# Kernel tuning notes

Hardware: AMD Instinct MI355X
Metric: run time of the kernel (lower is better)

The kernel has to match this reference:

```python
import jax, jax.numpy as jnp
import numpy as np

B, S, DIM = 2, 2048, 2048
N_HEADS, N_KV_HEADS = 16, 4
HEAD_DIM = DIM // N_HEADS  # 128
N_REP = N_HEADS // N_KV_HEADS  # 4
ROPE_THETA = 10000.0


def setup_inputs() -> dict:
    key = jax.random.key(0)
    ks = jax.random.split(key, 6)
    x = jax.random.normal(ks[0], (B, S, DIM), dtype=jnp.float32)
    # torch nn.Linear weights are [out_features, in_features]
    sc = 0.02
    wq = jax.random.normal(ks[1], (N_HEADS * HEAD_DIM, DIM), dtype=jnp.float32) * sc
    wk = jax.random.normal(ks[2], (N_KV_HEADS * HEAD_DIM, DIM), dtype=jnp.float32) * sc
    wv = jax.random.normal(ks[3], (N_KV_HEADS * HEAD_DIM, DIM), dtype=jnp.float32) * sc
    wo = jax.random.normal(ks[4], (DIM, N_HEADS * HEAD_DIM), dtype=jnp.float32) * sc
    # precomputed rotary table (freqs_cis in llama): [S, head_dim//2]
    inv_freq = 1.0 / (ROPE_THETA ** (jnp.arange(0, HEAD_DIM, 2, dtype=jnp.float32) / HEAD_DIM))
    t = jnp.arange(S, dtype=jnp.float32)
    freqs = jnp.outer(t, inv_freq)  # [S, head_dim//2]
    freqs_cos = jnp.cos(freqs)
    freqs_sin = jnp.sin(freqs)
    # additive causal mask as passed to SDPA (float, 0 on allowed, -inf-like elsewhere)
    causal = jnp.tril(jnp.ones((S, S), dtype=bool))
    mask = jnp.where(causal, 0.0, -1e9).astype(jnp.float32)
    return {"x": x, "wq": wq, "wk": wk, "wv": wv, "wo": wo,
            "freqs_cos": freqs_cos, "freqs_sin": freqs_sin, "mask": mask}


def _apply_rope(t, cos, sin):
    # t: [B, S, H, D]; cos/sin: [S, D//2] -> complex multiply on adjacent pairs
    tr = t.reshape(*t.shape[:-1], -1, 2)  # [B,S,H,D/2,2]
    tre, tim = tr[..., 0], tr[..., 1]
    c = cos[None, :, None, :]
    s = sin[None, :, None, :]
    out_re = tre * c - tim * s
    out_im = tre * s + tim * c
    return jnp.stack([out_re, out_im], axis=-1).reshape(t.shape)


def reference(x, wq, wk, wv, wo, freqs_cos, freqs_sin, mask):
    Bx, Sx, _ = x.shape
    xq = (x @ wq.T).reshape(Bx, Sx, N_HEADS, HEAD_DIM)
    xk = (x @ wk.T).reshape(Bx, Sx, N_KV_HEADS, HEAD_DIM)
    xv = (x @ wv.T).reshape(Bx, Sx, N_KV_HEADS, HEAD_DIM)
    xq = _apply_rope(xq, freqs_cos, freqs_sin)
    xk = _apply_rope(xk, freqs_cos, freqs_sin)
    # repeat_kv for GQA: [B,S,KV,D] -> [B,S,KV*n_rep,D]
    keys = jnp.repeat(xk, N_REP, axis=2)
    values = jnp.repeat(xv, N_REP, axis=2)
    q = xq.transpose(0, 2, 1, 3)      # [B,H,S,D]
    k = keys.transpose(0, 2, 1, 3)
    v = values.transpose(0, 2, 1, 3)
    scale = 1.0 / jnp.sqrt(jnp.float32(HEAD_DIM))
    scores = jnp.einsum('bhqd,bhkd->bhqk', q, k) * scale + mask[None, None]
    attn = jax.nn.softmax(scores, axis=-1)
    out = jnp.einsum('bhqk,bhkd->bhqd', attn, v)
    out = out.transpose(0, 2, 1, 3).reshape(Bx, Sx, -1)
    return out @ wo.T
```

## Files before the change

### kernel.cpp

```cpp
#include <hip/hip_runtime.h>
#include <hip/hip_bf16.h>

#define B_   2
#define S_   2048
#define DIM_ 2048
#define NH   16
#define NKV  4
#define HD   128
#define QKVN 3072

typedef __attribute__((ext_vector_type(8)))  short  sv8;
typedef __attribute__((ext_vector_type(8)))  ushort usv8;
typedef __attribute__((ext_vector_type(4)))  float  fv4;
typedef __attribute__((ext_vector_type(16))) float  fv16;

__device__ __forceinline__ float fast_exp2(float x) {
  return __builtin_amdgcn_exp2f(x);
}

__device__ __forceinline__ ushort f2bf(float f) {
  __hip_bfloat16 h = __float2bfloat16(f);
  union { __hip_bfloat16 h; ushort u; } c; c.h = h; return c.u;
}
__device__ __forceinline__ float bf2f(ushort u) {
  union { unsigned int i; float f; } c; c.i = ((unsigned)u) << 16; return c.f;
}

__device__ __forceinline__ unsigned int cvtpk(float lo, float hi) {
  unsigned int r;
  asm("v_cvt_pk_bf16_f32 %0, %1, %2" : "=v"(r) : "v"(lo), "v"(hi));
  return r;
}
__device__ __forceinline__ unsigned int xhalf(unsigned int x) {
  return (unsigned int)__shfl_xor((int)x, 32, 64);
}

__device__ __forceinline__ float tmax16(const fv16& v) {
  float a = fmaxf(fmaxf(v[0], v[1]),  fmaxf(v[2], v[3]));
  float b = fmaxf(fmaxf(v[4], v[5]),  fmaxf(v[6], v[7]));
  float c = fmaxf(fmaxf(v[8], v[9]),  fmaxf(v[10], v[11]));
  float d = fmaxf(fmaxf(v[12], v[13]), fmaxf(v[14], v[15]));
  return fmaxf(fmaxf(a, b), fmaxf(c, d));
}
__device__ __forceinline__ float tsum16(const fv16& v) {
  float a = (v[0] + v[1]) + (v[2] + v[3]);
  float b = (v[4] + v[5]) + (v[6] + v[7]);
  float c = (v[8] + v[9]) + (v[10] + v[11]);
  float d = (v[12] + v[13]) + (v[14] + v[15]);
  return (a + b) + (c + d);
}

__device__ __forceinline__ void async16(const void* g, void* l) {
  __builtin_amdgcn_global_load_lds(
      (const __attribute__((address_space(1))) unsigned int*)g,
      (__attribute__((address_space(3))) unsigned int*)l, 16, 0, 0);
}

__global__ void cvt_kernel(const float* __restrict__ in, ushort* __restrict__ out, int n) {
  int i = (blockIdx.x * 256 + threadIdx.x) * 4;
  if (i >= n) return;
  fv4 v = *(const fv4*)(in + i);
  ushort4 o;
  o.x = f2bf(v[0]); o.y = f2bf(v[1]); o.z = f2bf(v[2]); o.w = f2bf(v[3]);
  *(ushort4*)(out + i) = o;
}

__global__ void cvtw_kernel(const float* __restrict__ wq, const float* __restrict__ wk,
                            const float* __restrict__ wv, const float* __restrict__ wo,
                            ushort* __restrict__ wqkvb, ushort* __restrict__ wob) {
  const int NQ = 2048 * 2048, NK = 512 * 2048;
  int i = (blockIdx.x * 256 + threadIdx.x) * 4;
  const float* src; ushort* dst;
  if (i < NQ)               { src = wq + i;                 dst = wqkvb + i; }
  else if (i < NQ + NK)     { src = wk + (i - NQ);          dst = wqkvb + i; }
  else if (i < NQ + 2 * NK) { src = wv + (i - NQ - NK);     dst = wqkvb + i; }
  else                      { int j = i - (NQ + 2 * NK); src = wo + j; dst = wob + j; }
  fv4 v = *(const fv4*)src;
  ushort4 o;
  o.x = f2bf(v[0]); o.y = f2bf(v[1]); o.z = f2bf(v[2]); o.w = f2bf(v[3]);
  *(ushort4*)dst = o;
}

__global__ void rope2_kernel(const ushort* __restrict__ qkv, const float* __restrict__ fc,
                             const float* __restrict__ fs, ushort* __restrict__ qr,
                             ushort* __restrict__ kr, float qscale) {
  int t = blockIdx.x * 256 + threadIdx.x;
  int grp = t & 15;
  int u   = t >> 4;
  int h2  = u % 20;
  int s   = (u / 20) % S_;
  int b   = u / (20 * S_);
  bool isQ  = h2 < 16;
  int h     = isQ ? h2 : h2 - 16;
  int heads = isQ ? NH : NKV;
  float scale = isQ ? qscale : 1.0f;
  const ushort* src = qkv + (size_t)(b * S_ + s) * QKVN + (isQ ? 0 : 2048) + h * HD + grp * 8;
  sv8 v = *(const sv8*)src;
  fv4 c  = *(const fv4*)(fc + s * 64 + grp * 4);
  fv4 sn = *(const fv4*)(fs + s * 64 + grp * 4);
  sv8 o;
#pragma unroll
  for (int p = 0; p < 4; ++p) {
    float re = bf2f((ushort)v[2 * p]);
    float im = bf2f((ushort)v[2 * p + 1]);
    float orr = (re * c[p] - im * sn[p]) * scale;
    float oi  = (re * sn[p] + im * c[p]) * scale;
    o[2 * p]     = (short)f2bf(orr);
    o[2 * p + 1] = (short)f2bf(oi);
  }
  ushort* dst = (isQ ? qr : kr) + ((size_t)(b * heads + h) * S_ + s) * HD + grp * 8;
  *(sv8*)dst = o;
}

__global__ __launch_bounds__(256) void vtrans_kernel(const ushort* __restrict__ vraw,
                                                     ushort* __restrict__ vt, int rowstride) {
  __shared__ ushort tile[128][136];
  int blk = blockIdx.x;
  int st  = blk & 15;
  int kvb = blk >> 4;
  int kv  = kvb & 3;
  int b   = kvb >> 2;
  int s0  = st << 7;
#pragma unroll
  for (int it = 0; it < 8; ++it) {
    int t = it * 256 + threadIdx.x;
    int srow = t >> 4;
    int d8 = (t & 15) * 8;
    usv8 v = *(const usv8*)(vraw + (size_t)(b * S_ + s0 + srow) * rowstride + kv * HD + d8);
#pragma unroll
    for (int j = 0; j < 8; ++j) tile[d8 + j][srow] = v[j];
  }
  __syncthreads();
#pragma unroll
  for (int it = 0; it < 8; ++it) {
    int t = it * 256 + threadIdx.x;
    int d = t >> 4;
    int s8 = (t & 15) * 8;
    usv8 o;
#pragma unroll
    for (int j = 0; j < 8; ++j) o[j] = tile[d][s8 + j];
    *(usv8*)(vt + ((size_t)(b * NKV + kv) * HD + d) * S_ + s0 + s8) = o;
  }
}

template <typename OutT>
__global__ __launch_bounds__(512) void gemm192(const ushort* __restrict__ A,
                                               const ushort* __restrict__ Bm,
                                               OutT* __restrict__ C,
                                               int M, int N, int K) {
  __shared__ __align__(16) ushort SM[57344];
  int nb = N / 192;
  int bx = blockIdx.x % nb, by = blockIdx.x / nb;
  int m0 = by << 8;
  int n0 = bx * 192;
  int tid = threadIdx.x;
  int lane = tid & 63, w = tid >> 6;
  int l15 = lane & 15, lg = lane >> 4;
  int wm = (w >> 2) * 128;
  int wn = (w & 3) * 48;
  int pA = w >> 2;

  int srow = tid >> 3;
  int cb   = ((tid & 7) * 16) ^ ((srow & 7) << 4);
  const ushort* sA = A  + (size_t)(m0 + srow) * K + (cb >> 1);
  const ushort* sB = Bm + (size_t)(n0 + srow) * K + (cb >> 1);
  size_t rstep = (size_t)64 * K;
  int nkt = K >> 6;

  auto STG_A = [&](int t, int db) {
    ushort* base = SM + db * 28672 + (w << 9);
    const ushort* a0 = sA + (size_t)t * 64;
    async16(a0,             base);
    async16(a0 + rstep,     base + 4096);
    async16(a0 + 2 * rstep, base + 8192);
    async16(a0 + 3 * rstep, base + 12288);
  };
  auto STG_B = [&](int t, int db) {
    ushort* base = SM + db * 28672 + 16384 + (w << 9);
    const ushort* b0 = sB + (size_t)t * 64;
    async16(b0,             base);
    async16(b0 + rstep,     base + 4096);
    async16(b0 + 2 * rstep, base + 8192);
  };

  fv4 acc[8][3] = {};
  sv8 alo[4][2], ahi[4][2], b01[2][2], b2v[2];

  STG_A(0, 0); STG_B(0, 0);
  { int t1 = nkt > 1 ? 1 : 0; STG_A(t1, 1); STG_B(t1, 1); }
  asm volatile("s_waitcnt vmcnt(7)");
  __builtin_amdgcn_s_barrier();

  for (int t = 0; t < nkt; ++t) {
    int db = t & 1;
    int t2 = t + 2 < nkt ? t + 2 : nkt - 1;
    const char* Ab = (const char*)(SM + db * 28672) + pA * 16384;
    const char* Bb = (const char*)(SM + db * 28672) + 32768;

#pragma unroll
    for (int m = 0; m < 4; ++m)
#pragma unroll
      for (int kk = 0; kk < 2; ++kk) {
        int row = m * 16 + l15;
        alo[m][kk] = *(const sv8*)(Ab + row * 128 + ((kk * 64 + lg * 16) ^ ((row & 7) << 4)));
      }
#pragma unroll
    for (int m = 0; m < 4; ++m)
#pragma unroll
      for (int kk = 0; kk < 2; ++kk) {
        int row = 64 + m * 16 + l15;
        ahi[m][kk] = *(const sv8*)(Ab + row * 128 + ((kk * 64 + lg * 16) ^ ((row & 7) << 4)));
      }
#pragma unroll
    for (int j = 0; j < 2; ++j)
#pragma unroll
      for (int kk = 0; kk < 2; ++kk) {
        int row = wn + j * 16 + l15;
        b01[j][kk] = *(const sv8*)(Bb + row * 128 + ((kk * 64 + lg * 16) ^ ((row & 7) << 4)));
      }
#pragma unroll
    for (int kk = 0; kk < 2; ++kk) {
      int row = wn + 32 + l15;
      b2v[kk] = *(const sv8*)(Bb + row * 128 + ((kk * 64 + lg * 16) ^ ((row & 7) << 4)));
    }
    __builtin_amdgcn_s_barrier();
    asm volatile("s_waitcnt lgkmcnt(0)");
    __builtin_amdgcn_s_setprio(1);
#pragma unroll
    for (int m = 0; m < 4; ++m)
#pragma unroll
      for (int j = 0; j < 2; ++j)
#pragma unroll
        for (int kk = 0; kk < 2; ++kk) {
          acc[m][j]     = __builtin_amdgcn_mfma_f32_16x16x32_bf16(alo[m][kk], b01[j][kk], acc[m][j], 0, 0, 0);
          acc[m + 4][j] = __builtin_amdgcn_mfma_f32_16x16x32_bf16(ahi[m][kk], b01[j][kk], acc[m + 4][j], 0, 0, 0);
        }
    __builtin_amdgcn_s_setprio(0);
    __builtin_amdgcn_s_barrier();

    STG_A(t2, db);
    STG_B(t2, db);
    asm volatile("s_waitcnt vmcnt(7)");
    __builtin_amdgcn_s_barrier();
    __builtin_amdgcn_s_setprio(1);
#pragma unroll
    for (int m = 0; m < 4; ++m)
#pragma unroll
      for (int kk = 0; kk < 2; ++kk) {
        acc[m][2]     = __builtin_amdgcn_mfma_f32_16x16x32_bf16(alo[m][kk], b2v[kk], acc[m][2], 0, 0, 0);
        acc[m + 4][2] = __builtin_amdgcn_mfma_f32_16x16x32_bf16(ahi[m][kk], b2v[kk], acc[m + 4][2], 0, 0, 0);
      }
    __builtin_amdgcn_s_setprio(0);
    __builtin_amdgcn_s_barrier();
  }

  asm volatile("s_waitcnt vmcnt(0)");
#pragma unroll
  for (int m = 0; m < 8; ++m)
#pragma unroll
    for (int j = 0; j < 3; ++j)
#pragma unroll
      for (int r = 0; r < 4; ++r) {
        int row = m0 + wm + m * 16 + lg * 4 + r;
        int col = n0 + wn + j * 16 + l15;
        if constexpr (sizeof(OutT) == 2) C[(size_t)row * N + col] = (OutT)f2bf(acc[m][j][r]);
        else                             C[(size_t)row * N + col] = (OutT)acc[m][j][r];
      }
}

template <typename OutT>
__global__ __launch_bounds__(512) void gemmOP(const ushort* __restrict__ A,
                                              const ushort* __restrict__ Bm,
                                              OutT* __restrict__ C,
                                              int M, int N, int K) {
  __shared__ __align__(16) ushort SM[49152];
  int nb = N >> 7;
  int bx = blockIdx.x % nb, by = blockIdx.x / nb;
  int m0 = by << 8, n0 = bx << 7;
  int tid = threadIdx.x;
  int lane = tid & 63, w = tid >> 6;
  int l15 = lane & 15, lg = lane >> 4;
  int wm = (w >> 2) * 128;
  int wn = (w & 3) * 32;
  int pA = (w >> 2);

  int srow = tid >> 3;
  int cb   = ((tid & 7) * 16) ^ ((srow & 7) << 4);
  const ushort* sA0 = A  + (size_t)(m0 + srow) * K + (cb >> 1);
  const ushort* sB0 = Bm + (size_t)(n0 + srow) * K + (cb >> 1);
  const ushort* srcs[3] = { sA0, sA0 + (size_t)128 * K, sB0 };
  size_t rstep = (size_t)64 * K;

  int nkt = K >> 6;

  auto STG = [&](int part, int t, int db) {
    ushort* d0 = SM + db * 24576 + part * 8192 + (w << 9);
    const ushort* s0 = srcs[part] + t * 64;
    async16(s0, d0);
    async16(s0 + rstep, d0 + 4096);
  };

  fv4 acc[8][2] = {};
  sv8 a[8][2], b[2][2];

#pragma unroll
  for (int p = 0; p < 3; ++p) STG(p, 0, 0);
  {
    int t1 = 1 < nkt ? 1 : 0;
#pragma unroll
    for (int p = 0; p < 3; ++p) STG(p, t1, 1);
  }
  asm volatile("s_waitcnt vmcnt(6)");
  __builtin_amdgcn_s_barrier();

  for (int t = 0; t < nkt; ++t) {
    int db = t & 1;
    int t2 = t + 2 < nkt ? t + 2 : nkt - 1;
    const char* Ab = (const char*)SM + db * 49152 + pA * 16384;
    const char* Bb = (const char*)SM + db * 49152 + 32768;

#pragma unroll
    for (int m = 0; m < 8; ++m)
#pragma unroll
      for (int kk = 0; kk < 2; ++kk) {
        int row = m * 16 + l15;
        a[m][kk] = *(const sv8*)(Ab + row * 128 + ((kk * 64 + lg * 16) ^ ((row & 7) << 4)));
      }
#pragma unroll
    for (int j = 0; j < 2; ++j)
#pragma unroll
      for (int kk = 0; kk < 2; ++kk) {
        int row = wn + j * 16 + l15;
        b[j][kk] = *(const sv8*)(Bb + row * 128 + ((kk * 64 + lg * 16) ^ ((row & 7) << 4)));
      }
    __builtin_amdgcn_s_barrier();
    asm volatile("s_waitcnt lgkmcnt(0)");
    __builtin_amdgcn_s_setprio(1);
#pragma unroll
    for (int m = 0; m < 4; ++m)
#pragma unroll
      for (int j = 0; j < 2; ++j)
#pragma unroll
        for (int kk = 0; kk < 2; ++kk)
          acc[m][j] = __builtin_amdgcn_mfma_f32_16x16x32_bf16(a[m][kk], b[j][kk], acc[m][j], 0, 0, 0);
    __builtin_amdgcn_s_setprio(0);
    __builtin_amdgcn_s_barrier();

    STG(0, t2, db);
    STG(1, t2, db);
    STG(2, t2, db);
    asm volatile("s_waitcnt vmcnt(6)");
    __builtin_amdgcn_s_barrier();
    __builtin_amdgcn_s_setprio(1);
#pragma unroll
    for (int m = 0; m < 4; ++m)
#pragma unroll
      for (int j = 0; j < 2; ++j)
#pragma unroll
        for (int kk = 0; kk < 2; ++kk)
          acc[m + 4][j] = __builtin_amdgcn_mfma_f32_16x16x32_bf16(a[m + 4][kk], b[j][kk], acc[m + 4][j], 0, 0, 0);
    __builtin_amdgcn_s_setprio(0);
    __builtin_amdgcn_s_barrier();
  }

  asm volatile("s_waitcnt vmcnt(0)");
#pragma unroll
  for (int m = 0; m < 8; ++m)
#pragma unroll
    for (int j = 0; j < 2; ++j)
#pragma unroll
      for (int r = 0; r < 4; ++r) {
        int row = m0 + wm + m * 16 + lg * 4 + r;
        int col = n0 + wn + j * 16 + l15;
        if constexpr (sizeof(OutT) == 2) C[(size_t)row * N + col] = (OutT)f2bf(acc[m][j][r]);
        else                             C[(size_t)row * N + col] = (OutT)acc[m][j][r];
      }
}

__global__ __launch_bounds__(512, 2) void attn_kernel(const ushort* __restrict__ Q,
                                                      const ushort* __restrict__ Kr,
                                                      const ushort* __restrict__ Vt,
                                                      ushort* __restrict__ O) {
  __shared__ __align__(16) ushort SMEM[65536];

  int blk = blockIdx.x;
  int bh  = blk & 31;
  int pr  = blk >> 5;
  int h   = bh & 15;
  int b   = bh >> 4;
  int kv  = h >> 2;
  int lane = threadIdx.x & 63, w = threadIdx.x >> 6;
  int wg = w & 3, Hf = w >> 2;
  int l31 = lane & 31, hh = lane >> 5;

  const ushort* Qbase = Q  + (size_t)(b * NH  + h ) * S_ * HD;
  const ushort* Kbase = Kr + (size_t)(b * NKV + kv) * S_ * HD;
  const ushort* Vbase = Vt + (size_t)(b * NKV + kv) * HD * S_;

  const ushort* kSrc[4]; ushort* kDst[2][4];
  const ushort* vSrc[4]; ushort* vDst[2][4];
#pragma unroll
  for (int it = 0; it < 4; ++it) {
    int lin = it * 4096 + wg * 1024 + lane * 16;
    { int row = lin >> 8; int cbv = (lin & 255) ^ ((row & 15) << 4);
      kSrc[it] = Kbase + (size_t)row * HD + (cbv >> 1); }
    { int row = lin >> 8; int cp = lin & 255; int cl = cp ^ ((row & 15) << 4);
      int d = row + ((cl >> 7) << 6);
      int koff = (cl & 127) >> 1;
      vSrc[it] = Vbase + (size_t)d * S_ + koff; }
#pragma unroll
    for (int buf = 0; buf < 2; ++buf) {
      kDst[buf][it] = SMEM + Hf * 16384 + buf * 8192 + ((it * 4096 + wg * 1024) >> 1);
      vDst[buf][it] = SMEM + 32768 + Hf * 16384 + buf * 8192 + ((it * 4096 + wg * 1024) >> 1);
    }
  }

  float* cML = (float*)SMEM;
  float* cO  = (float*)SMEM + 512;

  for (int pass = 0; pass < 2; ++pass) {
    int qt = pass ? (15 - pr) : pr;
    int q0 = qt << 7;
    int qrow_w = q0 + wg * 32;
    int myq    = qrow_w + l31;
    int nj     = qt + 1;
    int ktbase = Hf * nj;

    sv8 qf[8];
#pragma unroll
    for (int kk = 0; kk < 8; ++kk)
      qf[kk] = *(const sv8*)(Qbase + (size_t)myq * HD + kk * 16 + hh * 8);

    fv16 oacc[4] = {};
    float mrun = -1e30f, lrun = 0.f;

    {
      size_t k0 = (size_t)ktbase << 6;
#pragma unroll
      for (int it = 0; it < 4; ++it) async16(kSrc[it] + k0 * HD, kDst[0][it]);
#pragma unroll
      for (int it = 0; it < 4; ++it) async16(vSrc[it] + k0,      vDst[0][it]);
    }

    for (int j = 0; j < nj; ++j) {
      int cur = j & 1, nxt = cur ^ 1;
      __syncthreads();
      if (j + 1 < nj) {
        size_t k0n = (size_t)(ktbase + j + 1) << 6;
#pragma unroll
        for (int it = 0; it < 4; ++it) async16(kSrc[it] + k0n * HD, kDst[nxt][it]);
#pragma unroll
        for (int it = 0; it < 4; ++it) async16(vSrc[it] + k0n,      vDst[nxt][it]);
      }
      const char* KsC = (const char*)(SMEM + Hf * 16384 + cur * 8192);
      const char* VsC = (const char*)(SMEM + 32768 + Hf * 16384 + cur * 8192);
      int k0 = (ktbase + j) << 6;

      fv16 sacc[2] = {};
      __builtin_amdgcn_s_setprio(1);
#pragma unroll
      for (int kk = 0; kk < 8; ++kk) {
        int cbq = kk * 32 + hh * 16;
        int r0 = l31, r1 = 32 + l31;
        sv8 kf0 = *(const sv8*)(KsC + r0 * 256 + (cbq ^ ((r0 & 15) << 4)));
        sv8 kf1 = *(const sv8*)(KsC + r1 * 256 + (cbq ^ ((r1 & 15) << 4)));
        sacc[0] = __builtin_amdgcn_mfma_f32_32x32x16_bf16(kf0, qf[kk], sacc[0], 0, 0, 0);
        sacc[1] = __builtin_amdgcn_mfma_f32_32x32x16_bf16(kf1, qf[kk], sacc[1], 0, 0, 0);
      }
      __builtin_amdgcn_s_setprio(0);

      if (k0 + 63 > qrow_w) {
        int thr = myq - k0 - 4 * hh;
#pragma unroll
        for (int t = 0; t < 2; ++t)
#pragma unroll
          for (int r = 0; r < 16; ++r) {
            int kp = t * 32 + (r & 3) + 8 * (r >> 2);
            if (kp > thr) sacc[t][r] = -1e38f;
          }
      }

      float tmax = fmaxf(tmax16(sacc[0]), tmax16(sacc[1]));
      tmax = fmaxf(tmax, __shfl_xor(tmax, 32, 64));

      if (__any(tmax > mrun + 8.0f)) {
        float mnew = fmaxf(mrun, tmax);
        float esc  = fast_exp2(mrun - mnew);
        lrun *= esc;
        float er[16];
#pragma unroll
        for (int r = 0; r < 16; ++r) er[r] = __shfl(esc, (r & 3) + 8 * (r >> 2) + 4 * hh, 64);
#pragma unroll
        for (int d0 = 0; d0 < 4; ++d0)
#pragma unroll
          for (int r = 0; r < 16; ++r) oacc[d0][r] *= er[r];
        mrun = mnew;
      }

#pragma unroll
      for (int t = 0; t < 2; ++t)
#pragma unroll
        for (int r = 0; r < 16; ++r) sacc[t][r] = fast_exp2(sacc[t][r] - mrun);
      float psum = tsum16(sacc[0]) + tsum16(sacc[1]);
      psum += __shfl_xor(psum, 32, 64);
      lrun += psum;

      union Frag { unsigned int u[4]; sv8 v; } pa[4];
#pragma unroll
      for (int t = 0; t < 2; ++t)
#pragma unroll
        for (int half = 0; half < 2; ++half) {
          int cbq = half * 8;
          unsigned int a0 = cvtpk(sacc[t][cbq + 0], sacc[t][cbq + 1]);
          unsigned int a1 = cvtpk(sacc[t][cbq + 2], sacc[t][cbq + 3]);
          unsigned int b0 = cvtpk(sacc[t][cbq + 4], sacc[t][cbq + 5]);
          unsigned int b1 = cvtpk(sacc[t][cbq + 6], sacc[t][cbq + 7]);
          unsigned int a0p = xhalf(a0), a1p = xhalf(a1);
          unsigned int b0p = xhalf(b0), b1p = xhalf(b1);
          pa[2 * t + half].u[0] = hh ? b0p : a0;
          pa[2 * t + half].u[1] = hh ? b1p : a1;
          pa[2 * t + half].u[2] = hh ? b0  : a0p;
          pa[2 * t + half].u[3] = hh ? b1  : a1p;
        }

      __builtin_amdgcn_s_setprio(1);
#pragma unroll
      for (int ks = 0; ks < 4; ++ks) {
#pragma unroll
        for (int d0 = 0; d0 < 4; ++d0) {
          int d = d0 * 32 + l31;
          int row = d & 63;
          int cl = ((d >> 6) << 7) + ks * 32 + hh * 16;
          sv8 vf = *(const sv8*)(VsC + row * 256 + (cl ^ ((row & 15) << 4)));
          oacc[d0] = __builtin_amdgcn_mfma_f32_32x32x16_bf16(pa[ks].v, vf, oacc[d0], 0, 0, 0);
        }
      }
      __builtin_amdgcn_s_setprio(0);
    }

    __syncthreads();
    if (Hf) {
      int base = wg * 64 + lane;
      cML[base * 2]     = mrun;
      cML[base * 2 + 1] = lrun;
      float* dst = cO + base * 65;
#pragma unroll
      for (int d0 = 0; d0 < 4; ++d0)
#pragma unroll
        for (int r = 0; r < 16; ++r) dst[d0 * 16 + r] = oacc[d0][r];
    }
    __syncthreads();
    if (!Hf) {
      int base = wg * 64 + lane;
      float m2 = cML[base * 2], l2 = cML[base * 2 + 1];
      const float* src = cO + base * 65;
      float m  = fmaxf(mrun, m2);
      float e1 = fast_exp2(mrun - m), e2 = fast_exp2(m2 - m);
      float l  = lrun * e1 + l2 * e2;
      float inv = 1.0f / l;
      float f1 = e1 * inv, f2 = e2 * inv;
      float f1b[16], f2b[16];
#pragma unroll
      for (int r = 0; r < 16; ++r) {
        int ro = (r & 3) + 8 * (r >> 2) + 4 * hh;
        f1b[r] = __shfl(f1, ro, 64);
        f2b[r] = __shfl(f2, ro, 64);
      }
#pragma unroll
      for (int r = 0; r < 16; ++r) {
        int q = qrow_w + (r & 3) + 8 * (r >> 2) + 4 * hh;
#pragma unroll
        for (int d0 = 0; d0 < 4; ++d0) {
          int d = d0 * 32 + l31;
          float val = oacc[d0][r] * f1b[r] + src[d0 * 16 + r] * f2b[r];
          O[(size_t)(b * S_ + q) * DIM_ + h * HD + d] = f2bf(val);
        }
      }
    }
    __syncthreads();
  }
}

extern "C" void kernel_launch(void* const* d_in, const int* in_sizes, int n_in,
                              void* d_out, int out_size, void* d_ws, size_t ws_size,
                              hipStream_t stream) {
  const float* x  = (const float*)d_in[0];
  const float* wq = (const float*)d_in[1];
  const float* wk = (const float*)d_in[2];
  const float* wv = (const float*)d_in[3];
  const float* wo = (const float*)d_in[4];
  const float* fc = (const float*)d_in[5];
  const float* fs = (const float*)d_in[6];
  float* out = (float*)d_out;

  char* ws = (char*)d_ws;
  size_t off = 0;
  auto alloc = [&](size_t bytes) -> ushort* {
    ushort* p = (ushort*)(ws + off);
    off += (bytes + 255) & ~(size_t)255;
    return p;
  };
  ushort* xb    = alloc((size_t)B_ * S_ * DIM_ * 2);
  ushort* wqkvb = alloc((size_t)QKVN * DIM_ * 2);
  ushort* wob   = alloc((size_t)DIM_ * DIM_ * 2);
  ushort* qkvr  = alloc((size_t)B_ * S_ * QKVN * 2);
  ushort* qr    = alloc((size_t)B_ * S_ * DIM_ * 2);
  ushort* kr    = alloc((size_t)B_ * S_ * NKV * HD * 2);
  ushort* vtb   = alloc((size_t)B_ * S_ * NKV * HD * 2);
  ushort* obf   = alloc((size_t)B_ * S_ * DIM_ * 2);
  (void)ws_size; (void)n_in; (void)in_sizes; (void)out_size;

  cvt_kernel<<<(B_ * S_ * DIM_) / 1024, 256, 0, stream>>>(x, xb, B_ * S_ * DIM_);
  cvtw_kernel<<<(2 * DIM_ * DIM_ + 2 * NKV * HD * DIM_) / 1024, 256, 0, stream>>>(
      wq, wk, wv, wo, wqkvb, wob);

  gemm192<ushort><<<(B_ * S_ / 256) * (QKVN / 192), 512, 0, stream>>>(xb, wqkvb, qkvr,
                                                                     B_ * S_, QKVN, DIM_);

  const float qscale = 0.08838834764831845f * 1.4426950408889634f;
  rope2_kernel<<<(B_ * S_ * 20 * 16) / 256, 256, 0, stream>>>(qkvr, fc, fs, qr, kr, qscale);
  vtrans_kernel<<<B_ * NKV * (S_ / 128), 256, 0, stream>>>(qkvr + 2560, vtb, QKVN);

  attn_kernel<<<B_ * NH * 8, 512, 0, stream>>>(qr, kr, vtb, obf);

  gemmOP<float><<<(B_ * S_ / 256) * (DIM_ / 128), 512, 0, stream>>>(obf, wob, out, B_ * S_, DIM_, DIM_);
}
```

Baseline: 186.2 us.

## Split heavy causal query tiles across blocks with atomic-counter global combine

```diff
diff --git a/kernel.cpp b/kernel.cpp
--- a/kernel.cpp
+++ b/kernel.cpp
@@ -377,21 +377,42 @@
       }
 }
 
-__global__ __launch_bounds__(512, 2) void attn_kernel(const ushort* __restrict__ Q,
+__global__ __launch_bounds__(256, 2) void attn_kernel(const ushort* __restrict__ Q,
                                                       const ushort* __restrict__ Kr,
                                                       const ushort* __restrict__ Vt,
-                                                      ushort* __restrict__ O) {
-  __shared__ __align__(16) ushort SMEM[65536];
-
-  int blk = blockIdx.x;
-  int bh  = blk & 31;
-  int pr  = blk >> 5;
+                                                      ushort* __restrict__ O,
+                                                      float* __restrict__ pOf,
+                                                      float* __restrict__ pML,
+                                                      int* __restrict__ cnt) {
+  __shared__ __align__(16) ushort SMEM[32768];
+  __shared__ int oldS;
+
+  int bid = blockIdx.x;
+  bool split = bid < 512;
+  int hf, key, qt, bh;
+  if (split) {
+    hf  = bid & 1;
+    key = bid >> 1;
+    bh  = key & 31;
+    qt  = 15 - (key >> 5);
+  } else {
+    hf  = 0;
+    key = 0;
+    int s = bid - 512;
+    bh  = s & 31;
+    qt  = 7 - (s >> 5);
+  }
   int h   = bh & 15;
   int b   = bh >> 4;
   int kv  = h >> 2;
-  int lane = threadIdx.x & 63, w = threadIdx.x >> 6;
-  int wg = w & 3, Hf = w >> 2;
+  int tid = threadIdx.x;
+  int lane = tid & 63, w = tid >> 6;
   int l31 = lane & 31, hh = lane >> 5;
+  int q0 = qt << 7;
+  int qrow_w = q0 + w * 32;
+  int myq    = qrow_w + l31;
+  int nj     = split ? (qt + 1) : (2 * qt + 2);
+  int ktbase = split ? hf * nj : 0;
 
   const ushort* Qbase = Q  + (size_t)(b * NH  + h ) * S_ * HD;
   const ushort* Kbase = Kr + (size_t)(b * NKV + kv) * S_ * HD;
@@ -401,7 +422,7 @@
   const ushort* vSrc[4]; ushort* vDst[2][4];
 #pragma unroll
   for (int it = 0; it < 4; ++it) {
-    int lin = it * 4096 + wg * 1024 + lane * 16;
+    int lin = it * 4096 + w * 1024 + lane * 16;
     { int row = lin >> 8; int cbv = (lin & 255) ^ ((row & 15) << 4);
       kSrc[it] = Kbase + (size_t)row * HD + (cbv >> 1); }
     { int row = lin >> 8; int cp = lin & 255; int cl = cp ^ ((row & 15) << 4);
@@ -410,174 +431,194 @@
       vSrc[it] = Vbase + (size_t)d * S_ + koff; }
 #pragma unroll
     for (int buf = 0; buf < 2; ++buf) {
-      kDst[buf][it] = SMEM + Hf * 16384 + buf * 8192 + ((it * 4096 + wg * 1024) >> 1);
-      vDst[buf][it] = SMEM + 32768 + Hf * 16384 + buf * 8192 + ((it * 4096 + wg * 1024) >> 1);
-    }
-  }
-
-  float* cML = (float*)SMEM;
-  float* cO  = (float*)SMEM + 512;
-
-  for (int pass = 0; pass < 2; ++pass) {
-    int qt = pass ? (15 - pr) : pr;
-    int q0 = qt << 7;
-    int qrow_w = q0 + wg * 32;
-    int myq    = qrow_w + l31;
-    int nj     = qt + 1;
-    int ktbase = Hf * nj;
-
-    sv8 qf[8];
-#pragma unroll
-    for (int kk = 0; kk < 8; ++kk)
-      qf[kk] = *(const sv8*)(Qbase + (size_t)myq * HD + kk * 16 + hh * 8);
-
-    fv16 oacc[4] = {};
-    float mrun = -1e30f, lrun = 0.f;
-
-    {
-      size_t k0 = (size_t)ktbase << 6;
-#pragma unroll
-      for (int it = 0; it < 4; ++it) async16(kSrc[it] + k0 * HD, kDst[0][it]);
-#pragma unroll
-      for (int it = 0; it < 4; ++it) async16(vSrc[it] + k0,      vDst[0][it]);
-    }
-
-    for (int j = 0; j < nj; ++j) {
-      int cur = j & 1, nxt = cur ^ 1;
-      __syncthreads();
-      if (j + 1 < nj) {
-        size_t k0n = (size_t)(ktbase + j + 1) << 6;
-#pragma unroll
-        for (int it = 0; it < 4; ++it) async16(kSrc[it] + k0n * HD, kDst[nxt][it]);
-#pragma unroll
-        for (int it = 0; it < 4; ++it) async16(vSrc[it] + k0n,      vDst[nxt][it]);
-      }
-      const char* KsC = (const char*)(SMEM + Hf * 16384 + cur * 8192);
-      const char* VsC = (const char*)(SMEM + 32768 + Hf * 16384 + cur * 8192);
-      int k0 = (ktbase + j) << 6;
-
-      fv16 sacc[2] = {};
-      __builtin_amdgcn_s_setprio(1);
-#pragma unroll
-      for (int kk = 0; kk < 8; ++kk) {
-        int cbq = kk * 32 + hh * 16;
-        int r0 = l31, r1 = 32 + l31;
-        sv8 kf0 = *(const sv8*)(KsC + r0 * 256 + (cbq ^ ((r0 & 15) << 4)));
-        sv8 kf1 = *(const sv8*)(KsC + r1 * 256 + (cbq ^ ((r1 & 15) << 4)));
-        sacc[0] = __builtin_amdgcn_mfma_f32_32x32x16_bf16(kf0, qf[kk], sacc[0], 0, 0, 0);
-        sacc[1] = __builtin_amdgcn_mfma_f32_32x32x16_bf16(kf1, qf[kk], sacc[1], 0, 0, 0);
-      }
-      __builtin_amdgcn_s_setprio(0);
-
-      if (k0 + 63 > qrow_w) {
-        int thr = myq - k0 - 4 * hh;
-#pragma unroll
-        for (int t = 0; t < 2; ++t)
-#pragma unroll
-          for (int r = 0; r < 16; ++r) {
-            int kp = t * 32 + (r & 3) + 8 * (r >> 2);
-            if (kp > thr) sacc[t][r] = -1e38f;
-          }
-      }
-
-      float tmax = fmaxf(tmax16(sacc[0]), tmax16(sacc[1]));
-      tmax = fmaxf(tmax, __shfl_xor(tmax, 32, 64));
-
-      if (__any(tmax > mrun + 8.0f)) {
-        float mnew = fmaxf(mrun, tmax);
-        float esc  = fast_exp2(mrun - mnew);
-        lrun *= esc;
-        float er[16];
-#pragma unroll
-        for (int r = 0; r < 16; ++r) er[r] = __shfl(esc, (r & 3) + 8 * (r >> 2) + 4 * hh, 64);
-#pragma unroll
-        for (int d0 = 0; d0 < 4; ++d0)
-#pragma unroll
-          for (int r = 0; r < 16; ++r) oacc[d0][r] *= er[r];
-        mrun = mnew;
-      }
-
+      kDst[buf][it] = SMEM + buf * 8192 + ((it * 4096 + w * 1024) >> 1);
+      vDst[buf][it] = SMEM + 16384 + buf * 8192 + ((it * 4096 + w * 1024) >> 1);
+    }
+  }
+
+  sv8 qf[8];
+#pragma unroll
+  for (int kk = 0; kk < 8; ++kk)
+    qf[kk] = *(const sv8*)(Qbase + (size_t)myq * HD + kk * 16 + hh * 8);
+
+  fv16 oacc[4] = {};
+  float mrun = -1e30f, lrun = 0.f;
+
+  {
+    size_t k0 = (size_t)ktbase << 6;
+#pragma unroll
+    for (int it = 0; it < 4; ++it) async16(kSrc[it] + k0 * HD, kDst[0][it]);
+#pragma unroll
+    for (int it = 0; it < 4; ++it) async16(vSrc[it] + k0,      vDst[0][it]);
+  }
+
+  for (int j = 0; j < nj; ++j) {
+    int cur = j & 1, nxt = cur ^ 1;
+    __syncthreads();
+    if (j + 1 < nj) {
+      size_t k0n = (size_t)(ktbase + j + 1) << 6;
+#pragma unroll
+      for (int it = 0; it < 4; ++it) async16(kSrc[it] + k0n * HD, kDst[nxt][it]);
+#pragma unroll
+      for (int it = 0; it < 4; ++it) async16(vSrc[it] + k0n,      vDst[nxt][it]);
+    }
+    const char* KsC = (const char*)(SMEM + cur * 8192);
+    const char* VsC = (const char*)(SMEM + 16384 + cur * 8192);
+    int k0 = (ktbase + j) << 6;
+
+    fv16 sacc[2] = {};
+    __builtin_amdgcn_s_setprio(1);
+#pragma unroll
+    for (int kk = 0; kk < 8; ++kk) {
+      int cbq = kk * 32 + hh * 16;
+      int r0 = l31, r1 = 32 + l31;
+      sv8 kf0 = *(const sv8*)(KsC + r0 * 256 + (cbq ^ ((r0 & 15) << 4)));
+      sv8 kf1 = *(const sv8*)(KsC + r1 * 256 + (cbq ^ ((r1 & 15) << 4)));
+      sacc[0] = __builtin_amdgcn_mfma_f32_32x32x16_bf16(kf0, qf[kk], sacc[0], 0, 0, 0);
+      sacc[1] = __builtin_amdgcn_mfma_f32_32x32x16_bf16(kf1, qf[kk], sacc[1], 0, 0, 0);
+    }
+    __builtin_amdgcn_s_setprio(0);
+
+    if (k0 + 63 > qrow_w) {
+      int thr = myq - k0 - 4 * hh;
 #pragma unroll
       for (int t = 0; t < 2; ++t)
 #pragma unroll
-        for (int r = 0; r < 16; ++r) sacc[t][r] = fast_exp2(sacc[t][r] - mrun);
-      float psum = tsum16(sacc[0]) + tsum16(sacc[1]);
-      psum += __shfl_xor(psum, 32, 64);
-      lrun += psum;
-
-      union Frag { unsigned int u[4]; sv8 v; } pa[4];
-#pragma unroll
-      for (int t = 0; t < 2; ++t)
-#pragma unroll
-        for (int half = 0; half < 2; ++half) {
-          int cbq = half * 8;
-          unsigned int a0 = cvtpk(sacc[t][cbq + 0], sacc[t][cbq + 1]);
-          unsigned int a1 = cvtpk(sacc[t][cbq + 2], sacc[t][cbq + 3]);
-          unsigned int b0 = cvtpk(sacc[t][cbq + 4], sacc[t][cbq + 5]);
-          unsigned int b1 = cvtpk(sacc[t][cbq + 6], sacc[t][cbq + 7]);
-          unsigned int a0p = xhalf(a0), a1p = xhalf(a1);
-          unsigned int b0p = xhalf(b0), b1p = xhalf(b1);
-          pa[2 * t + half].u[0] = hh ? b0p : a0;
-          pa[2 * t + half].u[1] = hh ? b1p : a1;
-          pa[2 * t + half].u[2] = hh ? b0  : a0p;
-          pa[2 * t + half].u[3] = hh ? b1  : a1p;
+        for (int r = 0; r < 16; ++r) {
+          int kp = t * 32 + (r & 3) + 8 * (r >> 2);
+          if (kp > thr) sacc[t][r] = -1e38f;
         }
-
-      __builtin_amdgcn_s_setprio(1);
-#pragma unroll
-      for (int ks = 0; ks < 4; ++ks) {
-#pragma unroll
-        for (int d0 = 0; d0 < 4; ++d0) {
-          int d = d0 * 32 + l31;
-          int row = d & 63;
-          int cl = ((d >> 6) << 7) + ks * 32 + hh * 16;
-          sv8 vf = *(const sv8*)(VsC + row * 256 + (cl ^ ((row & 15) << 4)));
-          oacc[d0] = __builtin_amdgcn_mfma_f32_32x32x16_bf16(pa[ks].v, vf, oacc[d0], 0, 0, 0);
-        }
-      }
-      __builtin_amdgcn_s_setprio(0);
-    }
-
-    __syncthreads();
-    if (Hf) {
-      int base = wg * 64 + lane;
-      cML[base * 2]     = mrun;
-      cML[base * 2 + 1] = lrun;
-      float* dst = cO + base * 65;
+    }
+
+    float tmax = fmaxf(tmax16(sacc[0]), tmax16(sacc[1]));
+    tmax = fmaxf(tmax, __shfl_xor(tmax, 32, 64));
+
+    if (__any(tmax > mrun + 8.0f)) {
+      float mnew = fmaxf(mrun, tmax);
+      float esc  = fast_exp2(mrun - mnew);
+      lrun *= esc;
+      float er[16];
+#pragma unroll
+      for (int r = 0; r < 16; ++r) er[r] = __shfl(esc, (r & 3) + 8 * (r >> 2) + 4 * hh, 64);
 #pragma unroll
       for (int d0 = 0; d0 < 4; ++d0)
 #pragma unroll
-        for (int r = 0; r < 16; ++r) dst[d0 * 16 + r] = oacc[d0][r];
-    }
-    __syncthreads();
-    if (!Hf) {
-      int base = wg * 64 + lane;
-      float m2 = cML[base * 2], l2 = cML[base * 2 + 1];
-      const float* src = cO + base * 65;
-      float m  = fmaxf(mrun, m2);
-      float e1 = fast_exp2(mrun - m), e2 = fast_exp2(m2 - m);
-      float l  = lrun * e1 + l2 * e2;
-      float inv = 1.0f / l;
-      float f1 = e1 * inv, f2 = e2 * inv;
-      float f1b[16], f2b[16];
-#pragma unroll
-      for (int r = 0; r < 16; ++r) {
-        int ro = (r & 3) + 8 * (r >> 2) + 4 * hh;
-        f1b[r] = __shfl(f1, ro, 64);
-        f2b[r] = __shfl(f2, ro, 64);
-      }
-#pragma unroll
-      for (int r = 0; r < 16; ++r) {
+        for (int r = 0; r < 16; ++r) oacc[d0][r] *= er[r];
+      mrun = mnew;
+    }
+
+#pragma unroll
+    for (int t = 0; t < 2; ++t)
+#pragma unroll
+      for (int r = 0; r < 16; ++r) sacc[t][r] = fast_exp2(sacc[t][r] - mrun);
+    float psum = tsum16(sacc[0]) + tsum16(sacc[1]);
+    psum += __shfl_xor(psum, 32, 64);
+    lrun += psum;
+
+    union Frag { unsigned int u[4]; sv8 v; } pa[4];
+#pragma unroll
+    for (int t = 0; t < 2; ++t)
+#pragma unroll
+      for (int half = 0; half < 2; ++half) {
+        int cbq = half * 8;
+        unsigned int a0 = cvtpk(sacc[t][cbq + 0], sacc[t][cbq + 1]);
+        unsigned int a1 = cvtpk(sacc[t][cbq + 2], sacc[t][cbq + 3]);
+        unsigned int b0 = cvtpk(sacc[t][cbq + 4], sacc[t][cbq + 5]);
+        unsigned int b1 = cvtpk(sacc[t][cbq + 6], sacc[t][cbq + 7]);
+        unsigned int a0p = xhalf(a0), a1p = xhalf(a1);
+        unsigned int b0p = xhalf(b0), b1p = xhalf(b1);
+        pa[2 * t + half].u[0] = hh ? b0p : a0;
+        pa[2 * t + half].u[1] = hh ? b1p : a1;
+        pa[2 * t + half].u[2] = hh ? b0  : a0p;
+        pa[2 * t + half].u[3] = hh ? b1  : a1p;
+      }
+
+    __builtin_amdgcn_s_setprio(1);
+#pragma unroll
+    for (int ks = 0; ks < 4; ++ks) {
+#pragma unroll
+      for (int d0 = 0; d0 < 4; ++d0) {
+        int d = d0 * 32 + l31;
+        int row = d & 63;
+        int cl = ((d >> 6) << 7) + ks * 32 + hh * 16;
+        sv8 vf = *(const sv8*)(VsC + row * 256 + (cl ^ ((row & 15) << 4)));
+        oacc[d0] = __builtin_amdgcn_mfma_f32_32x32x16_bf16(pa[ks].v, vf, oacc[d0], 0, 0, 0);
+      }
+    }
+    __builtin_amdgcn_s_setprio(0);
+  }
+
+  if (!split) {
+    float inv = 1.0f / lrun;
+    float ir[16];
+#pragma unroll
+    for (int r = 0; r < 16; ++r) ir[r] = __shfl(inv, (r & 3) + 8 * (r >> 2) + 4 * hh, 64);
+#pragma unroll
+    for (int r = 0; r < 16; ++r) {
+      int q = qrow_w + (r & 3) + 8 * (r >> 2) + 4 * hh;
+#pragma unroll
+      for (int d0 = 0; d0 < 4; ++d0) {
+        int d = d0 * 32 + l31;
+        O[(size_t)(b * S_ + q) * DIM_ + h * HD + d] = f2bf(oacc[d0][r] * ir[r]);
+      }
+    }
+    return;
+  }
+
+  {
+    float* myO = pOf + ((size_t)key * 2 + hf) * 16384 + (size_t)tid * 64;
+#pragma unroll
+    for (int d0 = 0; d0 < 4; ++d0)
+#pragma unroll
+      for (int j2 = 0; j2 < 4; ++j2) {
+        fv4 t;
+        t[0] = oacc[d0][4 * j2 + 0]; t[1] = oacc[d0][4 * j2 + 1];
+        t[2] = oacc[d0][4 * j2 + 2]; t[3] = oacc[d0][4 * j2 + 3];
+        *(fv4*)(myO + d0 * 16 + 4 * j2) = t;
+      }
+    float* myML = pML + ((size_t)key * 2 + hf) * 512 + tid * 2;
+    myML[0] = mrun;
+    myML[1] = lrun;
+  }
+  __threadfence();
+  __syncthreads();
+  if (tid == 0) oldS = atomicAdd(&cnt[key], 1);
+  __syncthreads();
+  if (oldS == 0) return;
+  __threadfence();
+
+  const float* o0 = pOf + (size_t)key * 32768 + (size_t)tid * 64;
+  const float* o1 = o0 + 16384;
+  const float* ml0 = pML + (size_t)key * 1024 + tid * 2;
+  const float* ml1 = ml0 + 512;
+  float m0 = ml0[0], l0 = ml0[1];
+  float m1 = ml1[0], l1 = ml1[1];
+  float mm = fmaxf(m0, m1);
+  float e0 = fast_exp2(m0 - mm), e1 = fast_exp2(m1 - mm);
+  float linv = 1.0f / (l0 * e0 + l1 * e1);
+  float f0 = e0 * linv, f1 = e1 * linv;
+  float f0b[16], f1b[16];
+#pragma unroll
+  for (int r = 0; r < 16; ++r) {
+    int ro = (r & 3) + 8 * (r >> 2) + 4 * hh;
+    f0b[r] = __shfl(f0, ro, 64);
+    f1b[r] = __shfl(f1, ro, 64);
+  }
+#pragma unroll
+  for (int d0 = 0; d0 < 4; ++d0) {
+#pragma unroll
+    for (int j2 = 0; j2 < 4; ++j2) {
+      fv4 x = *(const fv4*)(o0 + d0 * 16 + 4 * j2);
+      fv4 y = *(const fv4*)(o1 + d0 * 16 + 4 * j2);
+#pragma unroll
+      for (int rr = 0; rr < 4; ++rr) {
+        int r = 4 * j2 + rr;
+        float val = x[rr] * f0b[r] + y[rr] * f1b[r];
         int q = qrow_w + (r & 3) + 8 * (r >> 2) + 4 * hh;
-#pragma unroll
-        for (int d0 = 0; d0 < 4; ++d0) {
-          int d = d0 * 32 + l31;
-          float val = oacc[d0][r] * f1b[r] + src[d0 * 16 + r] * f2b[r];
-          O[(size_t)(b * S_ + q) * DIM_ + h * HD + d] = f2bf(val);
-        }
-      }
-    }
-    __syncthreads();
+        int d = d0 * 32 + l31;
+        O[(size_t)(b * S_ + q) * DIM_ + h * HD + d] = f2bf(val);
+      }
+    }
   }
 }
 
@@ -602,14 +643,18 @@
   };
   ushort* xb    = alloc((size_t)B_ * S_ * DIM_ * 2);
   ushort* wqkvb = alloc((size_t)QKVN * DIM_ * 2);
+  ushort* qkvr  = alloc((size_t)B_ * S_ * QKVN * 2);
   ushort* wob   = alloc((size_t)DIM_ * DIM_ * 2);
-  ushort* qkvr  = alloc((size_t)B_ * S_ * QKVN * 2);
   ushort* qr    = alloc((size_t)B_ * S_ * DIM_ * 2);
   ushort* kr    = alloc((size_t)B_ * S_ * NKV * HD * 2);
   ushort* vtb   = alloc((size_t)B_ * S_ * NKV * HD * 2);
   ushort* obf   = alloc((size_t)B_ * S_ * DIM_ * 2);
   (void)ws_size; (void)n_in; (void)in_sizes; (void)out_size;
 
+  float* pOf  = (float*)(ws + 0);
+  float* pML  = (float*)(ws + 33554432);
+  int*   cntP = (int*)(ws + 34603008);
+
   cvt_kernel<<<(B_ * S_ * DIM_) / 1024, 256, 0, stream>>>(x, xb, B_ * S_ * DIM_);
   cvtw_kernel<<<(2 * DIM_ * DIM_ + 2 * NKV * HD * DIM_) / 1024, 256, 0, stream>>>(
       wq, wk, wv, wo, wqkvb, wob);
@@ -621,7 +666,8 @@
   rope2_kernel<<<(B_ * S_ * 20 * 16) / 256, 256, 0, stream>>>(qkvr, fc, fs, qr, kr, qscale);
   vtrans_kernel<<<B_ * NKV * (S_ / 128), 256, 0, stream>>>(qkvr + 2560, vtb, QKVN);
 
-  attn_kernel<<<B_ * NH * 8, 512, 0, stream>>>(qr, kr, vtb, obf);
+  hipMemsetAsync(cntP, 0, 256 * sizeof(int), stream);
+  attn_kernel<<<768, 256, 0, stream>>>(qr, kr, vtb, obf, pOf, pML, cntP);
 
   gemmOP<float><<<(B_ * S_ / 256) * (DIM_ / 128), 512, 0, stream>>>(obf, wob, out, B_ * S_, DIM_, DIM_);
 }
```

Result: slower. 360.4 us (+93.6%).
